# Kernel optimization log

Hardware: AMD Instinct MI355X
Metric: run time of the kernel (lower is better)

Reference implementation:

```python
import jax, jax.numpy as jnp
import numpy as np


def rel_to_abs(x):
    """[b, hh, L, 2L-1] -> [b, hh, L, L] via pad/reshape trick."""
    b, hh, L, _ = x.shape
    x = jnp.pad(x, ((0, 0), (0, 0), (0, 0), (0, 1)))          # [b,hh,L,2L]
    flat = x.reshape(b, hh, L * 2 * L)
    flat = jnp.pad(flat, ((0, 0), (0, 0), (0, L - 1)))
    final = flat.reshape(b, hh, L + 1, 2 * L - 1)
    return final[:, :, :L, L - 1:]                             # [b,hh,L,L]


def relative_logits_1d(q, rel_k, transpose_mask):
    # q: [b, n, x, y, d]; rel_k: [2y-1, d]
    b, n, x, y, d = q.shape
    rel = jnp.einsum('bnxyd,md->bnxym', q, rel_k)
    rel = rel.reshape(b, n * x, y, 2 * y - 1)
    rel = rel_to_abs(rel)                                      # [b, n*x, y, y]
    rel = rel.reshape(b, n, x, y, y)
    rel = jnp.broadcast_to(rel[:, :, :, None, :, :], (b, n, x, x, y, y))
    return jnp.transpose(rel, transpose_mask)


def relative_logits(q, rel_emb_w, rel_emb_h):
    logits_w = relative_logits_1d(q, rel_emb_w, (0, 1, 2, 4, 3, 5))
    q_t = jnp.transpose(q, (0, 1, 3, 2, 4))  # swap h/w
    logits_h = relative_logits_1d(q_t, rel_emb_h, (0, 1, 4, 2, 5, 3))
    return logits_h + logits_w  # [b,n,h,w,h,w]


def setup_inputs() -> dict:
    key = jax.random.key(0)
    k1, k2, k3, k4, k5 = jax.random.split(key, 5)
    B, N, H, W, D = 4, 4, 48, 48, 32
    std = D ** (-0.5)
    return {
        'q': jax.random.normal(k1, (B, N, H, W, D), jnp.float32),
        'k': jax.random.normal(k2, (B, N, H, W, D), jnp.float32),
        'v': jax.random.normal(k3, (B, N, H, W, D), jnp.float32),
        'rel_emb_w': jax.random.normal(k4, (2 * W - 1, D), jnp.float32) * std,
        'rel_emb_h': jax.random.normal(k5, (2 * H - 1, D), jnp.float32) * std,
    }


def reference(q, k, v, rel_emb_w, rel_emb_h):
    bs, heads, h, w, dim = q.shape
    q = q * dim ** (-0.5)
    logits = jnp.einsum('bnhwd,bnpqd->bnhwpq', q, k)
    logits = logits + relative_logits(q, rel_emb_w, rel_emb_h)
    weights = jax.nn.softmax(logits.reshape(bs, heads, h, w, h * w), axis=-1)
    weights = weights.reshape(bs, heads, h, w, h, w)
    attn_out = jnp.einsum('bnhwpq,bnpqd->bhwnd', weights, v)
    # fold_heads=True
    return attn_out.reshape(bs, h, w, heads * dim)
```

## Files before the change

### kernel.cpp

```cpp
#include <hip/hip_runtime.h>
#include <hip/hip_bf16.h>


typedef __attribute__((ext_vector_type(8))) short bf16x8;
typedef __attribute__((ext_vector_type(4))) float f32x4;

#define DEVFN __device__ __forceinline__
#define AS1 __attribute__((address_space(1)))
#define AS3 __attribute__((address_space(3)))

#if __has_builtin(__builtin_amdgcn_exp2f)
#define EXP2(x) __builtin_amdgcn_exp2f(x)
#elif __has_builtin(__builtin_amdgcn_expf)
#define EXP2(x) __builtin_amdgcn_expf(x)
#else
#define EXP2(x) exp2f(x)
#endif

constexpr int H_ = 48, W_ = 48, D_ = 32;
constexpr int L_ = H_ * W_;
constexpr int BN_ = 16;

constexpr int QB2 = 48;
constexpr int KB2 = 96;
constexpr int IT2 = L_ / KB2;
constexpr int QT2 = L_ / QB2;
constexpr int NWG2 = BN_ * QT2;

constexpr size_t WE_Q = 0;
constexpr size_t WE_K = 1179648;
constexpr size_t WE_V = 2359296;
constexpr size_t WE_R = 3538944;
constexpr size_t WS_NEED = (WE_R + 2 * 6 * 64 * 8) * 2;

DEVFN unsigned short f2bf(float f) {
  unsigned u = __float_as_uint(f);
  return (unsigned short)((u + 0x7fffu + ((u >> 16) & 1u)) >> 16);
}
DEVFN unsigned pk2(float lo, float hi) {
  return (unsigned)f2bf(lo) | ((unsigned)f2bf(hi) << 16);
}
DEVFN unsigned pkcvt(float lo, float hi) {
  __hip_bfloat162 h = __float22bfloat162_rn(make_float2(lo, hi));
  union { __hip_bfloat162 h2; unsigned u; } cv; cv.h2 = h;
  return cv.u;
}
DEVFN void llds16(void* l, const void* g) {
  __builtin_amdgcn_global_load_lds((const AS1 unsigned*)g, (AS3 unsigned*)l, 16, 0, 0);
}

template <int CTRL>
DEVFN float dppf(float x) {
  return __int_as_float(__builtin_amdgcn_update_dpp(0, __float_as_int(x), CTRL, 0xF, 0xF, true));
}
DEVFN float rowmax16(float x) {
  x = fmaxf(x, dppf<0x128>(x));
  x = fmaxf(x, dppf<0x124>(x));
  x = fmaxf(x, dppf<0x122>(x));
  x = fmaxf(x, dppf<0x121>(x));
  return x;
}
DEVFN float rowsum16(float x) {
  x += dppf<0x128>(x);
  x += dppf<0x124>(x);
  x += dppf<0x122>(x);
  x += dppf<0x121>(x);
  return x;
}

__global__ __launch_bounds__(256)
void prep_kernel(const float* __restrict__ Q, const float* __restrict__ K,
                 const float* __restrict__ V, const float* __restrict__ RW,
                 const float* __restrict__ RH, unsigned short* __restrict__ ws)
{
  __shared__ __align__(16) float Vl[3072];
  const int bid = blockIdx.x, tid = threadIdx.x;
  const float QS = 0.17677669529663687f * 1.4426950408889634f;
  if (bid < 576) {
    size_t e = ((size_t)bid * 256 + tid) * 8;
    const float* s = Q + e;
    float4 a = *(const float4*)s, c = *(const float4*)(s + 4);
    uint4 wv;
    wv.x = pkcvt(a.x * QS, a.y * QS); wv.y = pkcvt(a.z * QS, a.w * QS);
    wv.z = pkcvt(c.x * QS, c.y * QS); wv.w = pkcvt(c.z * QS, c.w * QS);
    *(uint4*)(ws + WE_Q + e) = wv;
  } else if (bid < 1152) {
    int idx = (bid - 576) * 256 + tid;
    int lane = idx & 63, t = idx >> 6;
    int l15 = lane & 15, lg = lane >> 4;
    int bn = t / 144, t16 = t % 144;
    const float* s = K + ((size_t)(bn * L_ + t16 * 16 + l15) * D_ + lg * 8);
    float4 a = *(const float4*)s, c = *(const float4*)(s + 4);
    uint4 wv;
    wv.x = pkcvt(a.x, a.y); wv.y = pkcvt(a.z, a.w);
    wv.z = pkcvt(c.x, c.y); wv.w = pkcvt(c.z, c.w);
    *(uint4*)(ws + WE_K + (size_t)idx * 8) = wv;
  } else if (bid < 1536) {
    const int tile = bid - 1152;
    const float* src = V + (size_t)tile * 96 * D_;
    #pragma unroll
    for (int u = 0; u < 3; ++u)
      ((float4*)Vl)[tid + u * 256] = ((const float4*)src)[tid + u * 256];
    __syncthreads();
    unsigned short* dst = ws + WE_V + (size_t)tile * 3072;
    #pragma unroll
    for (int u = 0; u < 2; ++u) {
      const int f = tid + u * 256;
      if (f < 384) {
        const int sub = f >> 6, lane = f & 63;
        const int l15 = lane & 15, lg = lane >> 4;
        const int d  = (sub & 1) * 16 + l15;
        const int c0 = (sub >> 1) * 32 + lg * 8;
        float fv[8];
        #pragma unroll
        for (int j = 0; j < 8; ++j) {
          const int c = c0 + j;
          const int key = (c % 6) * 16 + c / 6;
          fv[j] = Vl[key * 32 + d];
        }
        uint4 wv;
        wv.x = pkcvt(fv[0], fv[1]); wv.y = pkcvt(fv[2], fv[3]);
        wv.z = pkcvt(fv[4], fv[5]); wv.w = pkcvt(fv[6], fv[7]);
        *(uint4*)(dst + (size_t)f * 8) = wv;
      }
    }
  } else {
    int t = (bid - 1536) * 256 + tid;
    if (t < 768) {
      int tbl = t / 384, rem = t % 384, jb = rem / 64, lane = rem % 64;
      int l15 = lane & 15, lg = lane >> 4;
      int j = jb * 16 + l15;
      int jc = (j > 94) ? 94 : j;
      const float* s = (tbl ? RW : RH) + jc * D_ + lg * 8;
      float4 a = *(const float4*)s, c = *(const float4*)(s + 4);
      uint4 wv;
      wv.x = pkcvt(a.x, a.y); wv.y = pkcvt(a.z, a.w);
      wv.z = pkcvt(c.x, c.y); wv.w = pkcvt(c.z, c.w);
      *(uint4*)(ws + WE_R + (size_t)t * 8) = wv;
    }
  }
}

__global__ __launch_bounds__(192, 2)
void relattn2(const unsigned short* __restrict__ ws, float* __restrict__ OUT)
{
  __shared__ __align__(16) char lds[44160];
  unsigned short* Kbase = (unsigned short*)lds;
  unsigned short* Vbase = (unsigned short*)(lds + 12288);
  unsigned short* Pl    = (unsigned short*)(lds + 24576);
  float* BhT = (float*)(lds + 34560);
  float* BwT = (float*)lds;

  const unsigned short* Qb = ws + WE_Q;
  const unsigned short* Kf = ws + WE_K;
  const unsigned short* Vf = ws + WE_V;
  const unsigned short* Rf = ws + WE_R;

  const int bid = blockIdx.x;
  const int wg  = (bid & 7) * (NWG2 / 8) + (bid >> 3);
  const int bn  = wg / QT2;
  const int qb  = (wg % QT2) * QB2;
  const int b   = bn >> 2, n = bn & 3;

  const int tid  = threadIdx.x;
  const int wave = tid >> 6;
  const int lane = tid & 63;
  const int l15  = lane & 15;
  const int lg   = lane >> 4;

  const int qi = qb + wave * 16 + l15;
  const bf16x8 qfrag = *(const bf16x8*)(Qb + (size_t)(bn * L_ + qi) * D_ + lg * 8);

  const f32x4 z4 = {0.f, 0.f, 0.f, 0.f};

  int hq[4], wq[4];
  #pragma unroll
  for (int r = 0; r < 4; ++r) {
    int qg = qb + wave * 16 + lg * 4 + r;
    hq[r] = qg / 48; wq[r] = qg % 48;
  }

  #pragma unroll
  for (int jb = 0; jb < 6; ++jb) {
    bf16x8 rhf = *(const bf16x8*)(Rf + ((0 * 6 + jb) * 64 + lane) * 8);
    bf16x8 rwf = *(const bf16x8*)(Rf + ((1 * 6 + jb) * 64 + lane) * 8);
    f32x4 mh = __builtin_amdgcn_mfma_f32_16x16x32_bf16(qfrag, rhf, z4, 0, 0, 0);
    f32x4 mw = __builtin_amdgcn_mfma_f32_16x16x32_bf16(qfrag, rwf, z4, 0, 0, 0);
    const int j = jb * 16 + l15;
    if (j < 95) {
      #pragma unroll
      for (int r = 0; r < 4; ++r) {
        const int row = wave * 16 + lg * 4 + r;
        const int p  = j - 47 + hq[r];
        if (p >= 0 && p < 48)  BhT[row * 50 + p]  = mh[r];
        const int ww = j - 47 + wq[r];
        if (ww >= 0 && ww < 48) BwT[row * 49 + ww] = mw[r];
      }
    }
  }
  float bw[3][4];
  #pragma unroll
  for (int x = 0; x < 3; ++x)
    #pragma unroll
    for (int r = 0; r < 4; ++r)
      bw[x][r] = BwT[(wave * 16 + lg * 4 + r) * 49 + x * 16 + l15];

  __syncthreads();

  const unsigned short* KfB = Kf + (size_t)bn * 24 * 3072;
  const unsigned short* VfB = Vf + (size_t)bn * 24 * 3072;

  auto stage = [&](int buf, int it) {
    const unsigned short* kt = KfB + (size_t)it * 3072;
    const unsigned short* vt = VfB + (size_t)it * 3072;
    char* kd = lds + buf * 6144;
    char* vd = lds + 12288 + buf * 6144;
    #pragma unroll
    for (int g2 = 0; g2 < 4; ++g2) {
      const int g = wave * 4 + g2;
      if (g < 6) llds16(kd + g * 1024, kt + g * 512 + lane * 8);
      else       llds16(vd + (g - 6) * 1024, vt + (g - 6) * 512 + lane * 8);
    }
  };

  f32x4 acc0 = z4, acc1 = z4;
  float l_r[4] = {0.f, 0.f, 0.f, 0.f};

  stage(0, 0);
  __syncthreads();
  int cur = 0;

  for (int it = 0; it < IT2; ++it) {
    if (it + 1 < IT2) stage(cur ^ 1, it + 1);

    const unsigned short* kb_ = Kbase + cur * 3072;
    const unsigned short* vb_ = Vbase + cur * 3072;

    float2 bhp[4];
    #pragma unroll
    for (int r = 0; r < 4; ++r)
      bhp[r] = *(const float2*)&BhT[(wave * 16 + lg * 4 + r) * 50 + it * 2];

    f32x4 sacc[6];
    #pragma unroll
    for (int kb = 0; kb < 6; ++kb) {
      f32x4 cin;
      #pragma unroll
      for (int r = 0; r < 4; ++r)
        cin[r] = (kb < 3 ? bhp[r].x : bhp[r].y) + bw[kb % 3][r];
      bf16x8 kf = *(const bf16x8*)(kb_ + (kb * 64 + lane) * 8);
      sacc[kb] = __builtin_amdgcn_mfma_f32_16x16x32_bf16(qfrag, kf, cin, 0, 0, 0);
    }

    #pragma unroll
    for (int r = 0; r < 4; ++r) {
      const float pe0 = EXP2(sacc[0][r]);
      const float pe1 = EXP2(sacc[1][r]);
      const float pe2 = EXP2(sacc[2][r]);
      const float pe3 = EXP2(sacc[3][r]);
      const float pe4 = EXP2(sacc[4][r]);
      const float pe5 = EXP2(sacc[5][r]);
      l_r[r] += ((pe0 + pe1) + (pe2 + pe3)) + (pe4 + pe5);
      unsigned short* pr = Pl + (wave * 16 + lg * 4 + r) * 104 + l15 * 6;
      *(unsigned*)(pr + 0) = pkcvt(pe0, pe1);
      *(unsigned*)(pr + 2) = pkcvt(pe2, pe3);
      *(unsigned*)(pr + 4) = pkcvt(pe4, pe5);
    }

    #pragma unroll
    for (int s3 = 0; s3 < 3; ++s3) {
      bf16x8 a2 = *(const bf16x8*)(Pl + (wave * 16 + l15) * 104 + s3 * 32 + lg * 8);
      bf16x8 b0 = *(const bf16x8*)(vb_ + ((s3 * 2 + 0) * 64 + lane) * 8);
      bf16x8 b1 = *(const bf16x8*)(vb_ + ((s3 * 2 + 1) * 64 + lane) * 8);
      acc0 = __builtin_amdgcn_mfma_f32_16x16x32_bf16(a2, b0, acc0, 0, 0, 0);
      acc1 = __builtin_amdgcn_mfma_f32_16x16x32_bf16(a2, b1, acc1, 0, 0, 0);
    }

    __syncthreads();
    cur ^= 1;
  }

  #pragma unroll
  for (int r = 0; r < 4; ++r) {
    const float lsum = rowsum16(l_r[r]);
    const float inv = __builtin_amdgcn_rcpf(lsum);
    float* op = OUT + ((size_t)(b * 48 + hq[r]) * 48 + wq[r]) * 128 + n * 32 + l15;
    op[0]  = acc0[r] * inv;
    op[16] = acc1[r] * inv;
  }
}

__global__ __launch_bounds__(256, 2)
void relattn_kernel(const float* __restrict__ Q, const float* __restrict__ K,
                    const float* __restrict__ V, const float* __restrict__ RW,
                    const float* __restrict__ RH, float* __restrict__ OUT)
{
  __shared__ __align__(16) unsigned short Klds[64][40];
  __shared__ __align__(16) unsigned       VT[32][36];
  __shared__ __align__(16) unsigned short Plds[4][16][72];
  __shared__ __align__(16) float          Bh[64][49];
  __shared__ __align__(16) float          Bw[64][49];

  const int bid = blockIdx.x;
  const int wg  = (bid & 7) * 72 + (bid >> 3);
  const int bn  = wg / 36;
  const int qb  = (wg % 36) * 64;
  const int b   = bn >> 2, n = bn & 3;

  const int tid  = threadIdx.x;
  const int wave = tid >> 6;
  const int lane = tid & 63;
  const int l15  = lane & 15;
  const int lg   = lane >> 4;

  const float QS = 0.17677669529663687f * 1.4426950408889634f;
  const int qi = qb + wave * 16 + l15;
  bf16x8 qfrag;
  {
    const float* qr = Q + ((bn * L_ + qi) * D_ + lg * 8);
    float4 a = *(const float4*)qr;
    float4 c = *(const float4*)(qr + 4);
    qfrag[0] = (short)f2bf(a.x * QS); qfrag[1] = (short)f2bf(a.y * QS);
    qfrag[2] = (short)f2bf(a.z * QS); qfrag[3] = (short)f2bf(a.w * QS);
    qfrag[4] = (short)f2bf(c.x * QS); qfrag[5] = (short)f2bf(c.y * QS);
    qfrag[6] = (short)f2bf(c.z * QS); qfrag[7] = (short)f2bf(c.w * QS);
  }
  const f32x4 z4 = {0.f, 0.f, 0.f, 0.f};
  #pragma unroll
  for (int jb = 0; jb < 6; ++jb) {
    const int j  = jb * 16 + l15;
    const int jc = (j > 94) ? 94 : j;
    bf16x8 rhf, rwf;
    {
      const float* rr = RH + jc * D_ + lg * 8;
      float4 a = *(const float4*)rr; float4 c = *(const float4*)(rr + 4);
      rhf[0] = (short)f2bf(a.x); rhf[1] = (short)f2bf(a.y);
      rhf[2] = (short)f2bf(a.z); rhf[3] = (short)f2bf(a.w);
      rhf[4] = (short)f2bf(c.x); rhf[5] = (short)f2bf(c.y);
      rhf[6] = (short)f2bf(c.z); rhf[7] = (short)f2bf(c.w);
      const float* rr2 = RW + jc * D_ + lg * 8;
      float4 a2 = *(const float4*)rr2; float4 c2 = *(const float4*)(rr2 + 4);
      rwf[0] = (short)f2bf(a2.x); rwf[1] = (short)f2bf(a2.y);
      rwf[2] = (short)f2bf(a2.z); rwf[3] = (short)f2bf(a2.w);
      rwf[4] = (short)f2bf(c2.x); rwf[5] = (short)f2bf(c2.y);
      rwf[6] = (short)f2bf(c2.z); rwf[7] = (short)f2bf(c2.w);
    }
    f32x4 mh = __builtin_amdgcn_mfma_f32_16x16x32_bf16(qfrag, rhf, z4, 0, 0, 0);
    f32x4 mw = __builtin_amdgcn_mfma_f32_16x16x32_bf16(qfrag, rwf, z4, 0, 0, 0);
    #pragma unroll
    for (int r = 0; r < 4; ++r) {
      const int qrow = lg * 4 + r;
      const int qg   = qb + wave * 16 + qrow;
      const int hqv  = qg / 48, wqv = qg % 48;
      if (j < 95) {
        const int p  = j - 47 + hqv;
        if (p >= 0 && p < 48) Bh[wave * 16 + qrow][p] = mh[r];
        const int ww = j - 47 + wqv;
        if (ww >= 0 && ww < 48) Bw[wave * 16 + qrow][ww] = mw[r];
      }
    }
  }
  float bw0[4], bw1[4], bw2[4];
  #pragma unroll
  for (int r = 0; r < 4; ++r) {
    bw0[r] = Bw[wave * 16 + lg * 4 + r][ 0 + l15];
    bw1[r] = Bw[wave * 16 + lg * 4 + r][16 + l15];
    bw2[r] = Bw[wave * 16 + lg * 4 + r][32 + l15];
  }
  f32x4 acc0 = z4, acc1 = z4;
  float m_r[4] = {-INFINITY, -INFINITY, -INFINITY, -INFINITY};
  float l_r[4] = {0.f, 0.f, 0.f, 0.f};
  const float* kbase = K + bn * L_ * D_;
  const float* vbase = V + bn * L_ * D_;
  for (int it = 0; it < 36; ++it) {
    const int kv0 = it * 64;
    __syncthreads();
    {
      const int r = tid >> 2, c = (tid & 3) * 8;
      const float* s = kbase + (kv0 + r) * D_ + c;
      float4 a = *(const float4*)s; float4 cc = *(const float4*)(s + 4);
      uint4 wv;
      wv.x = pk2(a.x, a.y);  wv.y = pk2(a.z, a.w);
      wv.z = pk2(cc.x, cc.y); wv.w = pk2(cc.z, cc.w);
      *(uint4*)&Klds[r][c] = wv;
    }
    {
      const int kp = tid >> 3, dg = tid & 7;
      const float* s0 = vbase + (kv0 + 2 * kp) * D_ + dg * 4;
      float4 a = *(const float4*)s0;
      float4 c = *(const float4*)(s0 + D_);
      VT[dg * 4 + 0][kp] = pk2(a.x, c.x);
      VT[dg * 4 + 1][kp] = pk2(a.y, c.y);
      VT[dg * 4 + 2][kp] = pk2(a.z, c.z);
      VT[dg * 4 + 3][kp] = pk2(a.w, c.w);
    }
    __syncthreads();
    f32x4 sacc[4];
    #pragma unroll
    for (int kb = 0; kb < 4; ++kb) {
      bf16x8 kf = *(const bf16x8*)&Klds[kb * 16 + l15][lg * 8];
      sacc[kb] = __builtin_amdgcn_mfma_f32_16x16x32_bf16(qfrag, kf, z4, 0, 0, 0);
    }
    const int p0   = kv0 / 48;
    const int tthr = (p0 + 1) * 48 - kv0;
    const int m0   = it % 3;
    float bh0[4], bh1[4];
    #pragma unroll
    for (int r = 0; r < 4; ++r) {
      bh0[r] = Bh[wave * 16 + lg * 4 + r][p0];
      bh1[r] = Bh[wave * 16 + lg * 4 + r][p0 + 1];
    }
    #pragma unroll
    for (int kb = 0; kb < 4; ++kb) {
      const bool hi = (kb * 16 + l15) >= tthr;
      int mm = m0 + kb; if (mm >= 3) mm -= 3; if (mm >= 3) mm -= 3;
      #pragma unroll
      for (int r = 0; r < 4; ++r) {
        const float bwv = (mm == 0) ? bw0[r] : ((mm == 1) ? bw1[r] : bw2[r]);
        sacc[kb][r] += (hi ? bh1[r] : bh0[r]) + bwv;
      }
    }
    #pragma unroll
    for (int r = 0; r < 4; ++r) {
      float mx = fmaxf(fmaxf(sacc[0][r], sacc[1][r]), fmaxf(sacc[2][r], sacc[3][r]));
      mx = rowmax16(mx);
      const float mn = fmaxf(m_r[r], mx);
      const float sc = exp2f(m_r[r] - mn);
      m_r[r] = mn;
      acc0[r] *= sc; acc1[r] *= sc;
      const float pe0 = exp2f(sacc[0][r] - mn);
      const float pe1 = exp2f(sacc[1][r] - mn);
      const float pe2 = exp2f(sacc[2][r] - mn);
      const float pe3 = exp2f(sacc[3][r] - mn);
      const float rs = rowsum16(pe0 + pe1 + pe2 + pe3);
      l_r[r] = l_r[r] * sc + rs;
      const int prow = lg * 4 + r;
      Plds[wave][prow][ 0 + l15] = f2bf(pe0);
      Plds[wave][prow][16 + l15] = f2bf(pe1);
      Plds[wave][prow][32 + l15] = f2bf(pe2);
      Plds[wave][prow][48 + l15] = f2bf(pe3);
    }
    const unsigned short* VTu = (const unsigned short*)VT;
    #pragma unroll
    for (int s2 = 0; s2 < 2; ++s2) {
      bf16x8 a2 = *(const bf16x8*)&Plds[wave][l15][s2 * 32 + lg * 8];
      bf16x8 b0 = *(const bf16x8*)&VTu[( 0 + l15) * 72 + s2 * 32 + lg * 8];
      bf16x8 b1 = *(const bf16x8*)&VTu[(16 + l15) * 72 + s2 * 32 + lg * 8];
      acc0 = __builtin_amdgcn_mfma_f32_16x16x32_bf16(a2, b0, acc0, 0, 0, 0);
      acc1 = __builtin_amdgcn_mfma_f32_16x16x32_bf16(a2, b1, acc1, 0, 0, 0);
    }
  }
  #pragma unroll
  for (int r = 0; r < 4; ++r) {
    const int qg = qb + wave * 16 + lg * 4 + r;
    const int hqv = qg / 48, wqv = qg % 48;
    const float inv = __builtin_amdgcn_rcpf(l_r[r]);
    float* op = OUT + ((b * 48 + hqv) * 48 + wqv) * 128 + n * 32 + l15;
    op[0]  = acc0[r] * inv;
    op[16] = acc1[r] * inv;
  }
}

extern "C" void kernel_launch(void* const* d_in, const int* in_sizes, int n_in,
                              void* d_out, int out_size, void* d_ws, size_t ws_size,
                              hipStream_t stream) {
  const float* q  = (const float*)d_in[0];
  const float* k  = (const float*)d_in[1];
  const float* v  = (const float*)d_in[2];
  const float* rw = (const float*)d_in[3];
  const float* rh = (const float*)d_in[4];
  float* out = (float*)d_out;
  if (ws_size >= WS_NEED) {
    unsigned short* ws = (unsigned short*)d_ws;
    hipLaunchKernelGGL(prep_kernel, dim3(1539), dim3(256), 0, stream, q, k, v, rw, rh, ws);
    hipLaunchKernelGGL(relattn2, dim3(NWG2), dim3(192), 0, stream, ws, out);
  } else {
    hipLaunchKernelGGL(relattn_kernel, dim3(576), dim3(256), 0, stream, q, k, v, rw, rh, out);
  }
}
```

Before: 50.88 us.

## Swap MFMA operands so softmax probabilities stay in registers, skipping LDS round-trip

New measurement: 46.79 us. -8.0%, faster.

```diff
diff --git a/kernel.cpp b/kernel.cpp
--- a/kernel.cpp
+++ b/kernel.cpp
@@ -11,8 +11,6 @@
 
 #if __has_builtin(__builtin_amdgcn_exp2f)
 #define EXP2(x) __builtin_amdgcn_exp2f(x)
-#elif __has_builtin(__builtin_amdgcn_expf)
-#define EXP2(x) __builtin_amdgcn_expf(x)
 #else
 #define EXP2(x) exp2f(x)
 #endif
@@ -89,7 +87,10 @@
     int lane = idx & 63, t = idx >> 6;
     int l15 = lane & 15, lg = lane >> 4;
     int bn = t / 144, t16 = t % 144;
-    const float* s = K + ((size_t)(bn * L_ + t16 * 16 + l15) * D_ + lg * 8);
+    int it = t16 / 6, kb = t16 % 6;
+    int kbp = kb >> 1, f = kb & 1;
+    int key96 = kbp * 32 + (l15 >> 2) * 8 + f * 4 + (l15 & 3);
+    const float* s = K + ((size_t)(bn * L_ + it * 96 + key96) * D_ + lg * 8);
     float4 a = *(const float4*)s, c = *(const float4*)(s + 4);
     uint4 wv;
     wv.x = pkcvt(a.x, a.y); wv.y = pkcvt(a.z, a.w);
@@ -105,23 +106,20 @@
     unsigned short* dst = ws + WE_V + (size_t)tile * 3072;
     #pragma unroll
     for (int u = 0; u < 2; ++u) {
-      const int f = tid + u * 256;
-      if (f < 384) {
-        const int sub = f >> 6, lane = f & 63;
+      const int f2i = tid + u * 256;
+      if (f2i < 384) {
+        const int f2 = f2i >> 6, lane = f2i & 63;
         const int l15 = lane & 15, lg = lane >> 4;
-        const int d  = (sub & 1) * 16 + l15;
-        const int c0 = (sub >> 1) * 32 + lg * 8;
+        const int kbp = f2 >> 1, half = f2 & 1;
+        const int d = half * 16 + l15;
         float fv[8];
         #pragma unroll
-        for (int j = 0; j < 8; ++j) {
-          const int c = c0 + j;
-          const int key = (c % 6) * 16 + c / 6;
-          fv[j] = Vl[key * 32 + d];
-        }
+        for (int j = 0; j < 8; ++j)
+          fv[j] = Vl[(kbp * 32 + lg * 8 + j) * 32 + d];
         uint4 wv;
         wv.x = pkcvt(fv[0], fv[1]); wv.y = pkcvt(fv[2], fv[3]);
         wv.z = pkcvt(fv[4], fv[5]); wv.w = pkcvt(fv[6], fv[7]);
-        *(uint4*)(dst + (size_t)f * 8) = wv;
+        *(uint4*)(dst + (size_t)f2i * 8) = wv;
       }
     }
   } else {
@@ -142,13 +140,12 @@
 }
 
 __global__ __launch_bounds__(192, 2)
-void relattn2(const unsigned short* __restrict__ ws, float* __restrict__ OUT)
+void relattn3(const unsigned short* __restrict__ ws, float* __restrict__ OUT)
 {
-  __shared__ __align__(16) char lds[44160];
+  __shared__ __align__(16) char lds[34176];
   unsigned short* Kbase = (unsigned short*)lds;
   unsigned short* Vbase = (unsigned short*)(lds + 12288);
-  unsigned short* Pl    = (unsigned short*)(lds + 24576);
-  float* BhT = (float*)(lds + 34560);
+  float* BhT = (float*)(lds + 24576);
   float* BwT = (float*)lds;
 
   const unsigned short* Qb = ws + WE_Q;
@@ -194,16 +191,22 @@
         const int p  = j - 47 + hq[r];
         if (p >= 0 && p < 48)  BhT[row * 50 + p]  = mh[r];
         const int ww = j - 47 + wq[r];
-        if (ww >= 0 && ww < 48) BwT[row * 49 + ww] = mw[r];
+        if (ww >= 0 && ww < 48) BwT[row * 52 + ww] = mw[r];
       }
     }
   }
-  float bw[3][4];
-  #pragma unroll
-  for (int x = 0; x < 3; ++x)
-    #pragma unroll
-    for (int r = 0; r < 4; ++r)
-      bw[x][r] = BwT[(wave * 16 + lg * 4 + r) * 49 + x * 16 + l15];
+
+  const int q52 = (wave * 16 + l15) * 52;
+  const int bt0 = lg * 8;
+  const int bt1 = (lg < 2) ? (lg * 8 + 32) : (lg * 8 - 16);
+  const int bt2 = lg * 8 + 16;
+  float bwv[3][8];
+  *(float4*)&bwv[0][0] = *(const float4*)&BwT[q52 + bt0];
+  *(float4*)&bwv[0][4] = *(const float4*)&BwT[q52 + bt0 + 4];
+  *(float4*)&bwv[1][0] = *(const float4*)&BwT[q52 + bt1];
+  *(float4*)&bwv[1][4] = *(const float4*)&BwT[q52 + bt1 + 4];
+  *(float4*)&bwv[2][0] = *(const float4*)&BwT[q52 + bt2];
+  *(float4*)&bwv[2][4] = *(const float4*)&BwT[q52 + bt2 + 4];
 
   __syncthreads();
 
@@ -224,7 +227,10 @@
   };
 
   f32x4 acc0 = z4, acc1 = z4;
-  float l_r[4] = {0.f, 0.f, 0.f, 0.f};
+  float l_acc = 0.f;
+
+  const float* bhrow = &BhT[(wave * 16 + l15) * 50];
+  const bool lglo = (lg < 2);
 
   stage(0, 0);
   __syncthreads();
@@ -236,58 +242,49 @@
     const unsigned short* kb_ = Kbase + cur * 3072;
     const unsigned short* vb_ = Vbase + cur * 3072;
 
-    float2 bhp[4];
-    #pragma unroll
-    for (int r = 0; r < 4; ++r)
-      bhp[r] = *(const float2*)&BhT[(wave * 16 + lg * 4 + r) * 50 + it * 2];
-
-    f32x4 sacc[6];
-    #pragma unroll
-    for (int kb = 0; kb < 6; ++kb) {
-      f32x4 cin;
+    const float2 bh2 = *(const float2*)(bhrow + it * 2);
+    const float bhm = lglo ? bh2.x : bh2.y;
+
+    #pragma unroll
+    for (int kbp = 0; kbp < 3; ++kbp) {
+      const float bhsel = (kbp == 0) ? bh2.x : ((kbp == 2) ? bh2.y : bhm);
+      f32x4 cin0, cin1;
       #pragma unroll
-      for (int r = 0; r < 4; ++r)
-        cin[r] = (kb < 3 ? bhp[r].x : bhp[r].y) + bw[kb % 3][r];
-      bf16x8 kf = *(const bf16x8*)(kb_ + (kb * 64 + lane) * 8);
-      sacc[kb] = __builtin_amdgcn_mfma_f32_16x16x32_bf16(qfrag, kf, cin, 0, 0, 0);
-    }
-
-    #pragma unroll
-    for (int r = 0; r < 4; ++r) {
-      const float pe0 = EXP2(sacc[0][r]);
-      const float pe1 = EXP2(sacc[1][r]);
-      const float pe2 = EXP2(sacc[2][r]);
-      const float pe3 = EXP2(sacc[3][r]);
-      const float pe4 = EXP2(sacc[4][r]);
-      const float pe5 = EXP2(sacc[5][r]);
-      l_r[r] += ((pe0 + pe1) + (pe2 + pe3)) + (pe4 + pe5);
-      unsigned short* pr = Pl + (wave * 16 + lg * 4 + r) * 104 + l15 * 6;
-      *(unsigned*)(pr + 0) = pkcvt(pe0, pe1);
-      *(unsigned*)(pr + 2) = pkcvt(pe2, pe3);
-      *(unsigned*)(pr + 4) = pkcvt(pe4, pe5);
-    }
-
-    #pragma unroll
-    for (int s3 = 0; s3 < 3; ++s3) {
-      bf16x8 a2 = *(const bf16x8*)(Pl + (wave * 16 + l15) * 104 + s3 * 32 + lg * 8);
-      bf16x8 b0 = *(const bf16x8*)(vb_ + ((s3 * 2 + 0) * 64 + lane) * 8);
-      bf16x8 b1 = *(const bf16x8*)(vb_ + ((s3 * 2 + 1) * 64 + lane) * 8);
-      acc0 = __builtin_amdgcn_mfma_f32_16x16x32_bf16(a2, b0, acc0, 0, 0, 0);
-      acc1 = __builtin_amdgcn_mfma_f32_16x16x32_bf16(a2, b1, acc1, 0, 0, 0);
+      for (int r = 0; r < 4; ++r) {
+        cin0[r] = bhsel + bwv[kbp][r];
+        cin1[r] = bhsel + bwv[kbp][4 + r];
+      }
+      bf16x8 kf0 = *(const bf16x8*)(kb_ + ((kbp * 2 + 0) * 64 + lane) * 8);
+      bf16x8 kf1 = *(const bf16x8*)(kb_ + ((kbp * 2 + 1) * 64 + lane) * 8);
+      f32x4 s0 = __builtin_amdgcn_mfma_f32_16x16x32_bf16(kf0, qfrag, cin0, 0, 0, 0);
+      f32x4 s1 = __builtin_amdgcn_mfma_f32_16x16x32_bf16(kf1, qfrag, cin1, 0, 0, 0);
+
+      const float e0 = EXP2(s0[0]), e1 = EXP2(s0[1]), e2 = EXP2(s0[2]), e3 = EXP2(s0[3]);
+      const float e4 = EXP2(s1[0]), e5 = EXP2(s1[1]), e6 = EXP2(s1[2]), e7 = EXP2(s1[3]);
+      l_acc += (((e0 + e1) + (e2 + e3)) + ((e4 + e5) + (e6 + e7)));
+      union { unsigned u[4]; bf16x8 v; } pf;
+      pf.u[0] = pkcvt(e0, e1); pf.u[1] = pkcvt(e2, e3);
+      pf.u[2] = pkcvt(e4, e5); pf.u[3] = pkcvt(e6, e7);
+
+      bf16x8 vf0 = *(const bf16x8*)(vb_ + ((kbp * 2 + 0) * 64 + lane) * 8);
+      bf16x8 vf1 = *(const bf16x8*)(vb_ + ((kbp * 2 + 1) * 64 + lane) * 8);
+      acc0 = __builtin_amdgcn_mfma_f32_16x16x32_bf16(vf0, pf.v, acc0, 0, 0, 0);
+      acc1 = __builtin_amdgcn_mfma_f32_16x16x32_bf16(vf1, pf.v, acc1, 0, 0, 0);
     }
 
     __syncthreads();
     cur ^= 1;
   }
 
-  #pragma unroll
-  for (int r = 0; r < 4; ++r) {
-    const float lsum = rowsum16(l_r[r]);
-    const float inv = __builtin_amdgcn_rcpf(lsum);
-    float* op = OUT + ((size_t)(b * 48 + hq[r]) * 48 + wq[r]) * 128 + n * 32 + l15;
-    op[0]  = acc0[r] * inv;
-    op[16] = acc1[r] * inv;
-  }
+  float ls = l_acc;
+  ls += __shfl_xor(ls, 16);
+  ls += __shfl_xor(ls, 32);
+  const float inv = __builtin_amdgcn_rcpf(ls);
+  const int ql = qb + wave * 16 + l15;
+  const int hql = ql / 48, wql = ql % 48;
+  float* op = OUT + ((size_t)(b * 48 + hql) * 48 + wql) * 128 + n * 32 + lg * 4;
+  *(float4*)op        = make_float4(acc0[0] * inv, acc0[1] * inv, acc0[2] * inv, acc0[3] * inv);
+  *(float4*)(op + 16) = make_float4(acc1[0] * inv, acc1[1] * inv, acc1[2] * inv, acc1[3] * inv);
 }
 
 __global__ __launch_bounds__(256, 2)
@@ -416,8 +413,8 @@
       int mm = m0 + kb; if (mm >= 3) mm -= 3; if (mm >= 3) mm -= 3;
       #pragma unroll
       for (int r = 0; r < 4; ++r) {
-        const float bwv = (mm == 0) ? bw0[r] : ((mm == 1) ? bw1[r] : bw2[r]);
-        sacc[kb][r] += (hi ? bh1[r] : bh0[r]) + bwv;
+        const float bwv2 = (mm == 0) ? bw0[r] : ((mm == 1) ? bw1[r] : bw2[r]);
+        sacc[kb][r] += (hi ? bh1[r] : bh0[r]) + bwv2;
       }
     }
     #pragma unroll
@@ -473,7 +470,7 @@
   if (ws_size >= WS_NEED) {
     unsigned short* ws = (unsigned short*)d_ws;
     hipLaunchKernelGGL(prep_kernel, dim3(1539), dim3(256), 0, stream, q, k, v, rw, rh, ws);
-    hipLaunchKernelGGL(relattn2, dim3(NWG2), dim3(192), 0, stream, ws, out);
+    hipLaunchKernelGGL(relattn3, dim3(NWG2), dim3(192), 0, stream, ws, out);
   } else {
     hipLaunchKernelGGL(relattn_kernel, dim3(576), dim3(256), 0, stream, q, k, v, rw, rh, out);
   }
```
